# Kernel tuning notes

Measured on AMD Instinct MI355X. Metric: run time of the kernel, lower is better.

## Reference

```python
import jax, jax.numpy as jnp
import numpy as np

NODES_PER_GRAPH = 32
NUM_GRAPHS = 4096
N = NUM_GRAPHS * NODES_PER_GRAPH  # 131072
DEG = 8
E = N * DEG
FEAT = 10


def setup_inputs() -> dict:
    key = jax.random.key(0)
    ks = jax.random.split(key, 32)
    x = jax.random.normal(ks[0], (N, FEAT), dtype=jnp.float32)
    src = jnp.repeat(jnp.arange(N, dtype=jnp.int64), DEG)
    dst = (src // NODES_PER_GRAPH) * NODES_PER_GRAPH + jax.random.randint(
        ks[1], (E,), 0, NODES_PER_GRAPH).astype(jnp.int64)
    edge_index = jnp.stack([src, dst])  # [2, E], row0 = source j, row1 = target i
    batch = (jnp.arange(N, dtype=jnp.int64) // NODES_PER_GRAPH)

    def lin(k, fan_in, shape):
        return jax.random.normal(k, shape, dtype=jnp.float32) / np.sqrt(fan_in)

    inp = dict(x=x, edge_index=edge_index, batch=batch)
    inp['Wq'] = lin(ks[2], 32, (32, 32))
    inp['Wk'] = lin(ks[3], 32, (32, 32))
    inp['Wv'] = lin(ks[4], 32, (32, 32))
    inp['W1'] = lin(ks[5], 10, (10, 64));  inp['a1s'] = lin(ks[6], 16, (4, 16))
    inp['a1d'] = lin(ks[7], 16, (4, 16));  inp['b1'] = jnp.zeros((64,), jnp.float32)
    inp['W2'] = lin(ks[8], 64, (64, 64));  inp['a2s'] = lin(ks[9], 16, (4, 16))
    inp['a2d'] = lin(ks[10], 16, (4, 16)); inp['b2'] = jnp.zeros((64,), jnp.float32)
    inp['W3'] = lin(ks[11], 64, (64, 64)); inp['a3s'] = lin(ks[12], 16, (4, 16))
    inp['a3d'] = lin(ks[13], 16, (4, 16)); inp['b3'] = jnp.zeros((64,), jnp.float32)
    inp['W4'] = lin(ks[14], 64, (64, 64)); inp['a4s'] = lin(ks[15], 64, (1, 64))
    inp['a4d'] = lin(ks[16], 64, (1, 64)); inp['b4'] = jnp.zeros((64,), jnp.float32)
    inp['fcW'] = lin(ks[17], 64, (64, 2)); inp['fcb'] = jnp.zeros((2,), jnp.float32)
    return inp


def gat_conv(x, src, dst, W, a_s, a_d, b, heads, out_c, concat):
    n = x.shape[0]
    h = (x @ W).reshape(n, heads, out_c)                    # [N,H,C]
    e_s = jnp.einsum('nhc,hc->nh', h, a_s)
    e_d = jnp.einsum('nhc,hc->nh', h, a_d)
    e = jax.nn.leaky_relu(e_s[src] + e_d[dst], 0.2)          # [E,H]
    e_max = jax.ops.segment_max(e, dst, num_segments=n)
    e = jnp.exp(e - e_max[dst])
    denom = jax.ops.segment_sum(e, dst, num_segments=n)
    alpha = e / (denom[dst] + 1e-16)                         # softmax per target node
    msg = h[src] * alpha[:, :, None]                         # [E,H,C]
    out = jax.ops.segment_sum(msg, dst, num_segments=n)      # [N,H,C]
    out = out.reshape(n, heads * out_c) if concat else out.mean(axis=1)
    return out + b


def forward(x, edge_index, batch, Wq, Wk, Wv, W1, a1s, a1d, b1, W2, a2s, a2d, b2,
            W3, a3s, a3d, b3, W4, a4s, a4d, b4, fcW, fcb):
    n = x.shape[0]
    b = n // NODES_PER_GRAPH
    # Attention_Layer1: (b*32, 10) -> (b, 10, 32)
    att_in = x.reshape(b, NODES_PER_GRAPH, FEAT).transpose(0, 2, 1)  # [b, sl=10, 32]
    Q = att_in @ Wq
    K = att_in @ Wk
    V = att_in @ Wv
    alpha = jax.nn.softmax(jnp.einsum('bsi,bti->bst', Q, K), axis=2)
    out = jnp.einsum('bst,bti->bsi', alpha, V)               # [b, 10, 32]
    # rearrange 'b i sl -> (b sl) i' with i=10, sl=32
    xg = out.transpose(0, 2, 1).reshape(n, FEAT)             # [(b*32), 10]
    # add self-loops (PyG GATConv default)
    loops = jnp.arange(n, dtype=edge_index.dtype)
    src = jnp.concatenate([edge_index[0], loops])
    dst = jnp.concatenate([edge_index[1], loops])
    xg = jax.nn.leaky_relu(gat_conv(xg, src, dst, W1, a1s, a1d, b1, 4, 16, True), 0.01)
    xg = jax.nn.leaky_relu(gat_conv(xg, src, dst, W2, a2s, a2d, b2, 4, 16, True), 0.01)
    xg = jax.nn.leaky_relu(gat_conv(xg, src, dst, W3, a3s, a3d, b3, 4, 16, True), 0.01)
    xg = jax.nn.leaky_relu(gat_conv(xg, src, dst, W4, a4s, a4d, b4, 1, 64, True), 0.01)
    # global mean pool per graph
    sums = jax.ops.segment_sum(xg, batch, num_segments=b)
    cnts = jax.ops.segment_sum(jnp.ones((n, 1), xg.dtype), batch, num_segments=b)
    pooled = sums / cnts                                     # [b, 64]
    logits = pooled @ fcW + fcb                              # [b, 2]
    probas = jax.nn.softmax(logits, axis=1)
    return logits, probas


def reference(x, edge_index, batch, Wq, Wk, Wv, W1, a1s, a1d, b1, W2, a2s, a2d, b2,
              W3, a3s, a3d, b3, W4, a4s, a4d, b4, fcW, fcb):
    return forward(x, edge_index, batch, Wq, Wk, Wv, W1, a1s, a1d, b1, W2, a2s, a2d,
                   b2, W3, a3s, a3d, b3, W4, a4s, a4d, b4, fcW, fcb)
```

## Files before the change

### kernel.cpp

```cpp
#include <hip/hip_runtime.h>


#define NGRAPH 4096
#define EDGES  (NGRAPH * 256)
#define NT     256
#define LOG2E  1.4426950408889634f

typedef __attribute__((ext_vector_type(8))) short bf16x8;
typedef __attribute__((ext_vector_type(4))) float f32x4;
typedef __attribute__((ext_vector_type(4))) int   i32x4;

__device__ __forceinline__ unsigned f2u(float x){ union{float f;unsigned u;}c;c.f=x;return c.u; }
__device__ __forceinline__ float u2f(unsigned u){ union{unsigned u;float f;}c;c.u=u;return c.f; }

__device__ __forceinline__ void split2(float x0, float x1, unsigned& dhi, unsigned& dlo){
    const unsigned u0 = f2u(x0), u1 = f2u(x1);
    dhi = (u0 >> 16) | (u1 & 0xffff0000u);
    const float l0 = x0 - u2f(u0 & 0xffff0000u);
    const float l1 = x1 - u2f(u1 & 0xffff0000u);
    dlo = (f2u(l0) >> 16) | (f2u(l1) & 0xffff0000u);
}

__device__ __forceinline__ f32x4 mfma16(i32x4 a, i32x4 b, f32x4 c){
    return __builtin_amdgcn_mfma_f32_16x16x32_bf16(
        __builtin_bit_cast(bf16x8, a), __builtin_bit_cast(bf16x8, b), c, 0, 0, 0);
}

template<int KSTEPS>
__device__ __forceinline__ void gat_layer(
    int tid,
    unsigned short (*xh_in)[72], unsigned short (*xl_in)[72],
    unsigned short (*xh_out)[72], unsigned short (*xl_out)[72],
    unsigned short* hh_w, unsigned short* hl_w, float* esw, float* edw,
    const unsigned int* Ap, const char* __restrict__ ws, int l,
    const float* __restrict__ b_g)
{
    const int lane = tid & 63, w = tid >> 6;
    const int n15 = lane & 15, q = lane >> 4;

    f32x4 hC0 = {0,0,0,0}, hC1 = {0,0,0,0};
    f32x4 eC0 = {0,0,0,0}, eC1 = {0,0,0,0};
#pragma unroll
    for (int ks = 0; ks < KSTEPS; ++ks){
        const unsigned short* wr = (const unsigned short*)(ws + l*16384)
                                   + (w*16 + n15)*64 + ks*32 + q*8;
        const i32x4 bh = *(const i32x4*)wr;
        const i32x4 bl = *(const i32x4*)(wr + 4096);
        const unsigned short* er = (const unsigned short*)(ws + 65536 + l*4096)
                                   + n15*64 + ks*32 + q*8;
        const i32x4 eh = *(const i32x4*)er;
        const i32x4 el = *(const i32x4*)(er + 1024);

        const i32x4 a0h = *(const i32x4*)&xh_in[n15][ks*32 + q*8];
        const i32x4 a0l = *(const i32x4*)&xl_in[n15][ks*32 + q*8];
        hC0 = mfma16(a0h, bh, hC0); hC0 = mfma16(a0h, bl, hC0); hC0 = mfma16(a0l, bh, hC0);
        eC0 = mfma16(a0h, eh, eC0); eC0 = mfma16(a0h, el, eC0); eC0 = mfma16(a0l, eh, eC0);

        const i32x4 a1h = *(const i32x4*)&xh_in[16 + n15][ks*32 + q*8];
        const i32x4 a1l = *(const i32x4*)&xl_in[16 + n15][ks*32 + q*8];
        hC1 = mfma16(a1h, bh, hC1); hC1 = mfma16(a1h, bl, hC1); hC1 = mfma16(a1l, bh, hC1);
        eC1 = mfma16(a1h, eh, eC1); eC1 = mfma16(a1h, el, eC1); eC1 = mfma16(a1l, eh, eC1);
    }

    if (n15 == 2*w || n15 == 2*w + 1){
        float* dst = (n15 & 1) ? edw : esw;
#pragma unroll
        for (int r = 0; r < 4; ++r){
            dst[q*4 + r]      = eC0[r];
            dst[16 + q*4 + r] = eC1[r];
        }
    }

#pragma unroll
    for (int mt = 0; mt < 2; ++mt){
        const f32x4 hv = mt ? hC1 : hC0;
        unsigned h0, l0v, h1, l1v;
        split2(hv[0], hv[1], h0, l0v);
        split2(hv[2], hv[3], h1, l1v);
        *(uint2*)&hh_w[n15*40 + mt*16 + q*4] = make_uint2(h0, h1);
        *(uint2*)&hl_w[n15*40 + mt*16 + q*4] = make_uint2(l0v, l1v);
    }

    float pf0[8], pf1[8];
    {
        float es8[8];
        *(float4*)&es8[0] = *(const float4*)&esw[q*8];
        *(float4*)&es8[4] = *(const float4*)&esw[q*8 + 4];
        const float ed0 = edw[n15], ed1 = edw[16 + n15];
        const uint2 c0 = make_uint2(Ap[n15*9 + 2*q], Ap[n15*9 + 2*q + 1]);
        const uint2 c1 = make_uint2(Ap[(16+n15)*9 + 2*q], Ap[(16+n15)*9 + 2*q + 1]);
        float ss0 = 0.f, ss1 = 0.f;
#pragma unroll
        for (int jj = 0; jj < 8; ++jj){
            const unsigned cnt0 = ((jj < 4 ? c0.x >> (8*jj) : c0.y >> (8*(jj-4))) & 0xffu);
            const unsigned cnt1 = ((jj < 4 ? c1.x >> (8*jj) : c1.y >> (8*(jj-4))) & 0xffu);
            float e0 = es8[jj] + ed0; e0 = fmaxf(e0, 0.2f*e0);
            float e1 = es8[jj] + ed1; e1 = fmaxf(e1, 0.2f*e1);
            const float p0 = (float)cnt0 * exp2f(e0);
            const float p1 = (float)cnt1 * exp2f(e1);
            pf0[jj] = p0; ss0 += p0;
            pf1[jj] = p1; ss1 += p1;
        }
        ss0 += __shfl_xor(ss0, 16); ss0 += __shfl_xor(ss0, 32);
        ss1 += __shfl_xor(ss1, 16); ss1 += __shfl_xor(ss1, 32);
        if (q == 0){
            edw[n15]      = 1.f/(ss0 + 1e-16f);
            edw[16 + n15] = 1.f/(ss1 + 1e-16f);
        }
    }

    {
        const i32x4 bh = *(const i32x4*)&hh_w[n15*40 + q*8];
        const i32x4 bl = *(const i32x4*)&hl_w[n15*40 + q*8];
        f32x4 o0 = {0,0,0,0}, o1 = {0,0,0,0};
        i32x4 ph, pl; unsigned th, tl;
#pragma unroll
        for (int r = 0; r < 4; ++r){
            split2(pf0[2*r], pf0[2*r+1], th, tl); ph[r] = (int)th; pl[r] = (int)tl;
        }
        o0 = mfma16(ph, bh, o0); o0 = mfma16(ph, bl, o0); o0 = mfma16(pl, bh, o0);
#pragma unroll
        for (int r = 0; r < 4; ++r){
            split2(pf1[2*r], pf1[2*r+1], th, tl); ph[r] = (int)th; pl[r] = (int)tl;
        }
        o1 = mfma16(ph, bh, o1); o1 = mfma16(ph, bl, o1); o1 = mfma16(pl, bh, o1);

        const float bv = __ldg(b_g + w*16 + n15);
        const f32x4 iv0 = *(const f32x4*)&edw[q*4];
        const f32x4 iv1 = *(const f32x4*)&edw[16 + q*4];
#pragma unroll
        for (int mt = 0; mt < 2; ++mt){
            const f32x4 ov = mt ? o1 : o0;
            const f32x4 iv = mt ? iv1 : iv0;
#pragma unroll
            for (int r = 0; r < 4; ++r){
                const int row = mt*16 + q*4 + r;
                float v = ov[r] * iv[r] + bv;
                v = fmaxf(v, 0.01f*v);
                const unsigned u = f2u(v);
                const float lo = v - u2f(u & 0xffff0000u);
                xh_out[row][w*16 + n15] = (unsigned short)(u >> 16);
                xl_out[row][w*16 + n15] = (unsigned short)(f2u(lo) >> 16);
            }
        }
    }
}

__global__ __launch_bounds__(NT) void gnn_fused(
    const float* __restrict__ x, const int* __restrict__ edge_index,
    const float* __restrict__ b1, const float* __restrict__ b2,
    const float* __restrict__ b3, const float* __restrict__ b4,
    const float* __restrict__ fcW, const float* __restrict__ fcb,
    const char* __restrict__ ws, float* __restrict__ out)
{
    __shared__ __align__(16) unsigned short xap[2][2][32][72];
    __shared__ __align__(16) unsigned short hT[4][2][16][40];
    __shared__ __align__(16) float es_l[4][32];
    __shared__ __align__(16) float ed_l[4][32];
    __shared__ __align__(16) unsigned int Ap[32*9];

    const int g = blockIdx.x, tid = threadIdx.x;
    const int lane = tid & 63, w = tid >> 6;
    const int n15 = lane & 15, q = lane >> 4;

    unsigned short* r0 = &xap[0][0][0][0];
    unsigned short* r1 = &hT[0][0][0][0];

    for (int idx = tid; idx < 288; idx += NT) Ap[idx] = 0u;
    for (int idx = tid; idx < 320; idx += NT){
        const int m = idx / 10, s = idx - 10*m;
        const float v = x[g*320 + idx];
        const unsigned u = f2u(v);
        const float lo = v - u2f(u & 0xffff0000u);
        r0[0   + s*40 + m] = (unsigned short)(u >> 16);
        r0[640 + s*40 + m] = (unsigned short)(f2u(lo) >> 16);
    }
    if (tid < 192){
        const int s = 10 + (tid >> 5), m = tid & 31;
        r0[0   + s*40 + m] = 0;
        r0[640 + s*40 + m] = 0;
    }
    __syncthreads();

    {
        const int* dstp = edge_index + EDGES + g*256;
        const int i = dstp[tid] & 31, j = tid >> 3;
        atomicAdd(&Ap[i*9 + (j >> 2)], 1u << (8*(j & 3)));
        if (tid < 32) atomicAdd(&Ap[tid*9 + (tid >> 2)], 1u << (8*(tid & 3)));
    }
    if (w < 3){
        const unsigned short* wb = (const unsigned short*)(ws + 81920 + w*4096);
        const i32x4 ah = *(const i32x4*)&r0[0   + n15*40 + q*8];
        const i32x4 al = *(const i32x4*)&r0[640 + n15*40 + q*8];
        f32x4 C0 = {0,0,0,0}, C1 = {0,0,0,0};
#pragma unroll
        for (int nt = 0; nt < 2; ++nt){
            const i32x4 bh = *(const i32x4*)&wb[(nt*16 + n15)*32 + q*8];
            const i32x4 bl = *(const i32x4*)&wb[1024 + (nt*16 + n15)*32 + q*8];
            f32x4 acc = nt ? C1 : C0;
            acc = mfma16(ah, bh, acc); acc = mfma16(ah, bl, acc); acc = mfma16(al, bh, acc);
            if (nt) C1 = acc; else C0 = acc;
        }
        if (w < 2){
            const int base = (w == 0) ? 1280 : 2560;
#pragma unroll
            for (int nt = 0; nt < 2; ++nt){
                const f32x4 cv = nt ? C1 : C0;
                const int i = nt*16 + n15;
#pragma unroll
                for (int r = 0; r < 4; ++r){
                    const int s = q*4 + r;
                    const float v = cv[r];
                    const unsigned u = f2u(v);
                    const float lo = v - u2f(u & 0xffff0000u);
                    r0[base + s*40 + i]       = (unsigned short)(u >> 16);
                    r0[base + 640 + s*40 + i] = (unsigned short)(f2u(lo) >> 16);
                }
            }
        } else {
#pragma unroll
            for (int nt = 0; nt < 2; ++nt){
                const f32x4 cv = nt ? C1 : C0;
                const int i = nt*16 + n15;
                unsigned h0, l0v, h1, l1v;
                split2(cv[0], cv[1], h0, l0v);
                split2(cv[2], cv[3], h1, l1v);
                *(uint2*)&r1[0    + i*40 + q*4] = make_uint2(h0, h1);
                *(uint2*)&r1[1280 + i*40 + q*4] = make_uint2(l0v, l1v);
            }
        }
    } else {
        const int plane = lane >> 5, row = lane & 31;
        unsigned short* dst = &r1[plane*1280 + row*40 + 16];
#pragma unroll
        for (int k = 0; k < 4; ++k) *(unsigned long long*)&dst[4*k] = 0ull;
    }
    __syncthreads();

    if (w == 0){
        const i32x4 ah = *(const i32x4*)&r0[1280 + n15*40 + q*8];
        const i32x4 al = *(const i32x4*)&r0[1920 + n15*40 + q*8];
        const i32x4 bh = *(const i32x4*)&r0[2560 + n15*40 + q*8];
        const i32x4 bl = *(const i32x4*)&r0[3200 + n15*40 + q*8];
        f32x4 Sc = {0,0,0,0};
        Sc = mfma16(ah, bh, Sc); Sc = mfma16(ah, bl, Sc); Sc = mfma16(al, bh, Sc);
        const bool valid = (n15 < 10);
#pragma unroll
        for (int r = 0; r < 4; ++r){
            float v = valid ? Sc[r] : -1e30f;
            float m = v;
            m = fmaxf(m, __shfl_xor(m, 1)); m = fmaxf(m, __shfl_xor(m, 2));
            m = fmaxf(m, __shfl_xor(m, 4)); m = fmaxf(m, __shfl_xor(m, 8));
            float p = valid ? exp2f((Sc[r] - m)*LOG2E) : 0.f;
            float s = p;
            s += __shfl_xor(s, 1); s += __shfl_xor(s, 2);
            s += __shfl_xor(s, 4); s += __shfl_xor(s, 8);
            const float sp = p / s;
            const int srow = q*4 + r;
            const unsigned u = f2u(sp);
            const float lo = sp - u2f(u & 0xffff0000u);
            r1[2560 + srow*40 + n15] = (unsigned short)(u >> 16);
            r1[3200 + srow*40 + n15] = (unsigned short)(f2u(lo) >> 16);
            r1[2560 + srow*40 + 16 + n15] = 0;
            r1[3200 + srow*40 + 16 + n15] = 0;
        }
    }
    __syncthreads();

    if (w < 2){
        const i32x4 ah = *(const i32x4*)&r1[2560 + n15*40 + q*8];
        const i32x4 al = *(const i32x4*)&r1[3200 + n15*40 + q*8];
        const i32x4 bh = *(const i32x4*)&r1[0    + (w*16 + n15)*40 + q*8];
        const i32x4 bl = *(const i32x4*)&r1[1280 + (w*16 + n15)*40 + q*8];
        f32x4 O = {0,0,0,0};
        O = mfma16(ah, bh, O); O = mfma16(ah, bl, O); O = mfma16(al, bh, O);
        const int ig = w*16 + n15;
#pragma unroll
        for (int r = 0; r < 4; ++r){
            const int s = q*4 + r;
            if (s < 10){
                const float v = O[r];
                const unsigned u = f2u(v);
                const float lo = v - u2f(u & 0xffff0000u);
                xap[0][0][ig][s] = (unsigned short)(u >> 16);
                xap[0][1][ig][s] = (unsigned short)(f2u(lo) >> 16);
            }
        }
    } else {
        const int idx = tid - 128;
        const int plane = idx >> 6, row = (idx >> 1) & 31, half = idx & 1;
        unsigned short* rowp = &xap[0][plane][row][0];
        if (half == 0){
            *(unsigned*)&rowp[10] = 0u;
#pragma unroll
            for (int c = 0; c < 6; ++c) *(unsigned long long*)&rowp[12 + 4*c] = 0ull;
        } else {
#pragma unroll
            for (int c = 0; c < 7; ++c) *(unsigned long long*)&rowp[36 + 4*c] = 0ull;
        }
    }
    __syncthreads();

    unsigned short* hh_w = &hT[w][0][0][0];
    unsigned short* hl_w = &hT[w][1][0][0];
    float* esw = es_l[w];
    float* edw = ed_l[w];
    gat_layer<1>(tid, xap[0][0], xap[0][1], xap[1][0], xap[1][1], hh_w, hl_w, esw, edw, Ap, ws, 0, b1);
    __syncthreads();
    gat_layer<2>(tid, xap[1][0], xap[1][1], xap[0][0], xap[0][1], hh_w, hl_w, esw, edw, Ap, ws, 1, b2);
    __syncthreads();
    gat_layer<2>(tid, xap[0][0], xap[0][1], xap[1][0], xap[1][1], hh_w, hl_w, esw, edw, Ap, ws, 2, b3);
    __syncthreads();
    gat_layer<2>(tid, xap[1][0], xap[1][1], xap[0][0], xap[0][1], hh_w, hl_w, esw, edw, Ap, ws, 3, b4);
    __syncthreads();

    if (tid < 64){
        float acc = 0.f;
#pragma unroll
        for (int n = 0; n < 32; ++n)
            acc += u2f(((unsigned)xap[0][0][n][tid]) << 16) + u2f(((unsigned)xap[0][1][n][tid]) << 16);
        const float p = acc*(1.f/32.f);
        float c0 = p*__ldg(fcW + 2*tid);
        float c1 = p*__ldg(fcW + 2*tid + 1);
#pragma unroll
        for (int off = 32; off > 0; off >>= 1){
            c0 += __shfl_down(c0, off);
            c1 += __shfl_down(c1, off);
        }
        if (tid == 0){
            const float l0 = c0 + __ldg(fcb), l1 = c1 + __ldg(fcb + 1);
            const float m = fmaxf(l0, l1);
            const float e0 = __expf(l0 - m), e1 = __expf(l1 - m);
            const float inv = 1.f/(e0 + e1);
            out[2*g] = l0;
            out[2*g + 1] = l1;
            out[2*NGRAPH + 2*g] = e0*inv;
            out[2*NGRAPH + 2*g + 1] = e1*inv;
        }
    }
}

__global__ void prep(
    const float* __restrict__ W1, const float* __restrict__ W2,
    const float* __restrict__ W3, const float* __restrict__ W4,
    const float* __restrict__ a1s, const float* __restrict__ a1d,
    const float* __restrict__ a2s, const float* __restrict__ a2d,
    const float* __restrict__ a3s, const float* __restrict__ a3d,
    const float* __restrict__ a4s, const float* __restrict__ a4d,
    const float* __restrict__ Wq, const float* __restrict__ Wk,
    const float* __restrict__ Wv,
    char* __restrict__ ws)
{
    const int b = blockIdx.x, tid = threadIdx.x;
    const float* Wl[4] = {W1, W2, W3, W4};
    const int Kl[4] = {10, 64, 64, 64};
    if (b < 32){
        const int l = b >> 3;
        const float* W = Wl[l];
        const int K = Kl[l];
        unsigned short* hi = (unsigned short*)(ws + l*16384);
        unsigned short* lo = hi + 4096;
        const int base = (b & 7)*512;
        for (int idx = base + tid; idx < base + 512; idx += NT){
            const int n = idx >> 6, k = idx & 63;
            const float v = (k < K) ? __ldg(W + k*64 + n) : 0.f;
            const unsigned u = f2u(v);
            const float lof = v - u2f(u & 0xffff0000u);
            hi[idx] = (unsigned short)(u >> 16);
            lo[idx] = (unsigned short)(f2u(lof) >> 16);
        }
    } else if (b < 36){
        const int l = b - 32;
        const float* W = Wl[l];
        const int K = Kl[l];
        const float* asp[4] = {a1s, a2s, a3s, a4s};
        const float* adp[4] = {a1d, a2d, a3d, a4d};
        const int C = (l < 3) ? 16 : 64;
        unsigned short* basep = (unsigned short*)(ws + 65536 + l*4096);
        for (int idx = tid; idx < 1024; idx += NT){
            const int n = idx >> 6, k = idx & 63;
            float val = 0.f;
            if (n < 8 && k < K){
                const int hh = (l < 3) ? (n >> 1) : 0;
                const float* av = (n & 1) ? adp[l] : asp[l];
                float s = 0.f;
                for (int c = 0; c < C; ++c)
                    s += __ldg(W + k*64 + hh*C + c) * __ldg(av + hh*C + c);
                val = s * LOG2E;
            }
            const unsigned u = f2u(val);
            const float lof = val - u2f(u & 0xffff0000u);
            basep[idx]        = (unsigned short)(u >> 16);
            basep[1024 + idx] = (unsigned short)(f2u(lof) >> 16);
        }
    } else {
        const int mat = b - 36;
        const float* W = (mat == 0) ? Wq : ((mat == 1) ? Wk : Wv);
        unsigned short* hi = (unsigned short*)(ws + 81920 + mat*4096);
        unsigned short* lo = hi + 1024;
        for (int idx = tid; idx < 1024; idx += NT){
            const int i = idx >> 5, m = idx & 31;
            const float v = __ldg(W + m*32 + i);
            const unsigned u = f2u(v);
            const float lof = v - u2f(u & 0xffff0000u);
            hi[idx] = (unsigned short)(u >> 16);
            lo[idx] = (unsigned short)(f2u(lof) >> 16);
        }
    }
}

extern "C" void kernel_launch(void* const* d_in, const int* in_sizes, int n_in,
                              void* d_out, int out_size, void* d_ws, size_t ws_size,
                              hipStream_t stream) {
    (void)in_sizes; (void)n_in; (void)ws_size; (void)out_size;
    prep<<<39, NT, 0, stream>>>(
        (const float*)d_in[6], (const float*)d_in[10], (const float*)d_in[14], (const float*)d_in[18],
        (const float*)d_in[7], (const float*)d_in[8],
        (const float*)d_in[11], (const float*)d_in[12],
        (const float*)d_in[15], (const float*)d_in[16],
        (const float*)d_in[19], (const float*)d_in[20],
        (const float*)d_in[3], (const float*)d_in[4], (const float*)d_in[5],
        (char*)d_ws);
    gnn_fused<<<NGRAPH, NT, 0, stream>>>(
        (const float*)d_in[0], (const int*)d_in[1],
        (const float*)d_in[9], (const float*)d_in[13], (const float*)d_in[17], (const float*)d_in[21],
        (const float*)d_in[22], (const float*)d_in[23],
        (const char*)d_ws, (float*)d_out);
}
```

Before: 200.5 us.

## Process one graph per wavefront, removing block-wide barriers

Changes the work split so each 64-lane wavefront handles a whole graph, with four graphs per 256-thread block, instead of four wavefronts sharing one graph. Each wave now computes all four head tiles of every GAT layer and the whole attention preamble on its own, so every __syncthreads is gone and shared-memory state becomes per-wave. The adjacency count packing also moves from 8-bit to 4-bit fields to shrink the per-graph shared footprint. The cost is more serial MFMA work and more registers per wave, plus a small risk of count overflow if a node has more than 15 duplicate edges to the same neighbour.

```diff
diff --git a/kernel.cpp b/kernel.cpp
--- a/kernel.cpp
+++ b/kernel.cpp
@@ -4,6 +4,7 @@
 #define NGRAPH 4096
 #define EDGES  (NGRAPH * 256)
 #define NT     256
+#define GPB    4
 #define LOG2E  1.4426950408889634f
 
 typedef __attribute__((ext_vector_type(8))) short bf16x8;
@@ -28,90 +29,104 @@
 
 template<int KSTEPS>
 __device__ __forceinline__ void gat_layer(
-    int tid,
-    unsigned short (*xh_in)[72], unsigned short (*xl_in)[72],
-    unsigned short (*xh_out)[72], unsigned short (*xl_out)[72],
-    unsigned short* hh_w, unsigned short* hl_w, float* esw, float* edw,
+    int lane, unsigned short* sw, float* esb, float* edb,
     const unsigned int* Ap, const char* __restrict__ ws, int l,
     const float* __restrict__ b_g)
 {
-    const int lane = tid & 63, w = tid >> 6;
     const int n15 = lane & 15, q = lane >> 4;
-
-    f32x4 hC0 = {0,0,0,0}, hC1 = {0,0,0,0};
+    unsigned short* xaH = sw;
+    unsigned short* xaL = sw + 2304;
+    unsigned short* hTH = sw + 4608;
+    unsigned short* hTL = sw + 5248;
+
+    f32x4 hC0[4], hC1[4];
     f32x4 eC0 = {0,0,0,0}, eC1 = {0,0,0,0};
 #pragma unroll
+    for (int nt = 0; nt < 4; ++nt){
+        hC0[nt] = (f32x4){0,0,0,0};
+        hC1[nt] = (f32x4){0,0,0,0};
+    }
+#pragma unroll
     for (int ks = 0; ks < KSTEPS; ++ks){
-        const unsigned short* wr = (const unsigned short*)(ws + l*16384)
-                                   + (w*16 + n15)*64 + ks*32 + q*8;
-        const i32x4 bh = *(const i32x4*)wr;
-        const i32x4 bl = *(const i32x4*)(wr + 4096);
+        const i32x4 a0h = *(const i32x4*)&xaH[n15*72 + ks*32 + q*8];
+        const i32x4 a0l = *(const i32x4*)&xaL[n15*72 + ks*32 + q*8];
+        const i32x4 a1h = *(const i32x4*)&xaH[(16+n15)*72 + ks*32 + q*8];
+        const i32x4 a1l = *(const i32x4*)&xaL[(16+n15)*72 + ks*32 + q*8];
+
         const unsigned short* er = (const unsigned short*)(ws + 65536 + l*4096)
                                    + n15*64 + ks*32 + q*8;
         const i32x4 eh = *(const i32x4*)er;
         const i32x4 el = *(const i32x4*)(er + 1024);
-
-        const i32x4 a0h = *(const i32x4*)&xh_in[n15][ks*32 + q*8];
-        const i32x4 a0l = *(const i32x4*)&xl_in[n15][ks*32 + q*8];
-        hC0 = mfma16(a0h, bh, hC0); hC0 = mfma16(a0h, bl, hC0); hC0 = mfma16(a0l, bh, hC0);
         eC0 = mfma16(a0h, eh, eC0); eC0 = mfma16(a0h, el, eC0); eC0 = mfma16(a0l, eh, eC0);
-
-        const i32x4 a1h = *(const i32x4*)&xh_in[16 + n15][ks*32 + q*8];
-        const i32x4 a1l = *(const i32x4*)&xl_in[16 + n15][ks*32 + q*8];
-        hC1 = mfma16(a1h, bh, hC1); hC1 = mfma16(a1h, bl, hC1); hC1 = mfma16(a1l, bh, hC1);
         eC1 = mfma16(a1h, eh, eC1); eC1 = mfma16(a1h, el, eC1); eC1 = mfma16(a1l, eh, eC1);
-    }
-
-    if (n15 == 2*w || n15 == 2*w + 1){
-        float* dst = (n15 & 1) ? edw : esw;
+
+#pragma unroll
+        for (int nt = 0; nt < 4; ++nt){
+            const unsigned short* wr = (const unsigned short*)(ws + l*16384)
+                                       + (nt*16 + n15)*64 + ks*32 + q*8;
+            const i32x4 bh = *(const i32x4*)wr;
+            const i32x4 bl = *(const i32x4*)(wr + 4096);
+            hC0[nt] = mfma16(a0h, bh, hC0[nt]);
+            hC0[nt] = mfma16(a0h, bl, hC0[nt]);
+            hC0[nt] = mfma16(a0l, bh, hC0[nt]);
+            hC1[nt] = mfma16(a1h, bh, hC1[nt]);
+            hC1[nt] = mfma16(a1h, bl, hC1[nt]);
+            hC1[nt] = mfma16(a1l, bh, hC1[nt]);
+        }
+    }
+
+    if (n15 < 8){
+        float* dst = (n15 & 1) ? edb : esb;
+        const int h = n15 >> 1;
 #pragma unroll
         for (int r = 0; r < 4; ++r){
-            dst[q*4 + r]      = eC0[r];
-            dst[16 + q*4 + r] = eC1[r];
-        }
-    }
-
-#pragma unroll
-    for (int mt = 0; mt < 2; ++mt){
-        const f32x4 hv = mt ? hC1 : hC0;
-        unsigned h0, l0v, h1, l1v;
-        split2(hv[0], hv[1], h0, l0v);
-        split2(hv[2], hv[3], h1, l1v);
-        *(uint2*)&hh_w[n15*40 + mt*16 + q*4] = make_uint2(h0, h1);
-        *(uint2*)&hl_w[n15*40 + mt*16 + q*4] = make_uint2(l0v, l1v);
-    }
-
-    float pf0[8], pf1[8];
-    {
-        float es8[8];
-        *(float4*)&es8[0] = *(const float4*)&esw[q*8];
-        *(float4*)&es8[4] = *(const float4*)&esw[q*8 + 4];
-        const float ed0 = edw[n15], ed1 = edw[16 + n15];
-        const uint2 c0 = make_uint2(Ap[n15*9 + 2*q], Ap[n15*9 + 2*q + 1]);
-        const uint2 c1 = make_uint2(Ap[(16+n15)*9 + 2*q], Ap[(16+n15)*9 + 2*q + 1]);
-        float ss0 = 0.f, ss1 = 0.f;
-#pragma unroll
-        for (int jj = 0; jj < 8; ++jj){
-            const unsigned cnt0 = ((jj < 4 ? c0.x >> (8*jj) : c0.y >> (8*(jj-4))) & 0xffu);
-            const unsigned cnt1 = ((jj < 4 ? c1.x >> (8*jj) : c1.y >> (8*(jj-4))) & 0xffu);
-            float e0 = es8[jj] + ed0; e0 = fmaxf(e0, 0.2f*e0);
-            float e1 = es8[jj] + ed1; e1 = fmaxf(e1, 0.2f*e1);
-            const float p0 = (float)cnt0 * exp2f(e0);
-            const float p1 = (float)cnt1 * exp2f(e1);
-            pf0[jj] = p0; ss0 += p0;
-            pf1[jj] = p1; ss1 += p1;
-        }
-        ss0 += __shfl_xor(ss0, 16); ss0 += __shfl_xor(ss0, 32);
-        ss1 += __shfl_xor(ss1, 16); ss1 += __shfl_xor(ss1, 32);
-        if (q == 0){
-            edw[n15]      = 1.f/(ss0 + 1e-16f);
-            edw[16 + n15] = 1.f/(ss1 + 1e-16f);
-        }
-    }
-
-    {
-        const i32x4 bh = *(const i32x4*)&hh_w[n15*40 + q*8];
-        const i32x4 bl = *(const i32x4*)&hl_w[n15*40 + q*8];
+            dst[h*32 + q*4 + r]      = eC0[r];
+            dst[h*32 + 16 + q*4 + r] = eC1[r];
+        }
+    }
+
+#pragma unroll
+    for (int nt = 0; nt < 4; ++nt){
+#pragma unroll
+        for (int mt = 0; mt < 2; ++mt){
+            const f32x4 hv = mt ? hC1[nt] : hC0[nt];
+            unsigned h0, l0v, h1, l1v;
+            split2(hv[0], hv[1], h0, l0v);
+            split2(hv[2], hv[3], h1, l1v);
+            *(uint2*)&hTH[n15*40 + mt*16 + q*4] = make_uint2(h0, h1);
+            *(uint2*)&hTL[n15*40 + mt*16 + q*4] = make_uint2(l0v, l1v);
+        }
+
+        float pf0[8], pf1[8];
+        {
+            float es8[8];
+            *(float4*)&es8[0] = *(const float4*)&esb[nt*32 + q*8];
+            *(float4*)&es8[4] = *(const float4*)&esb[nt*32 + q*8 + 4];
+            const float ed0 = edb[nt*32 + n15], ed1 = edb[nt*32 + 16 + n15];
+            const unsigned c0w = Ap[n15*5 + q];
+            const unsigned c1w = Ap[(16+n15)*5 + q];
+            float ss0 = 0.f, ss1 = 0.f;
+#pragma unroll
+            for (int jj = 0; jj < 8; ++jj){
+                const unsigned cnt0 = (c0w >> (4*jj)) & 0xfu;
+                const unsigned cnt1 = (c1w >> (4*jj)) & 0xfu;
+                float e0 = es8[jj] + ed0; e0 = fmaxf(e0, 0.2f*e0);
+                float e1 = es8[jj] + ed1; e1 = fmaxf(e1, 0.2f*e1);
+                const float p0 = (float)cnt0 * exp2f(e0);
+                const float p1 = (float)cnt1 * exp2f(e1);
+                pf0[jj] = p0; ss0 += p0;
+                pf1[jj] = p1; ss1 += p1;
+            }
+            ss0 += __shfl_xor(ss0, 16); ss0 += __shfl_xor(ss0, 32);
+            ss1 += __shfl_xor(ss1, 16); ss1 += __shfl_xor(ss1, 32);
+            if (q == 0){
+                edb[nt*32 + n15]      = 1.f/(ss0 + 1e-16f);
+                edb[nt*32 + 16 + n15] = 1.f/(ss1 + 1e-16f);
+            }
+        }
+
+        const i32x4 bh = *(const i32x4*)&hTH[n15*40 + q*8];
+        const i32x4 bl = *(const i32x4*)&hTL[n15*40 + q*8];
         f32x4 o0 = {0,0,0,0}, o1 = {0,0,0,0};
         i32x4 ph, pl; unsigned th, tl;
 #pragma unroll
@@ -125,9 +140,9 @@
         }
         o1 = mfma16(ph, bh, o1); o1 = mfma16(ph, bl, o1); o1 = mfma16(pl, bh, o1);
 
-        const float bv = __ldg(b_g + w*16 + n15);
-        const f32x4 iv0 = *(const f32x4*)&edw[q*4];
-        const f32x4 iv1 = *(const f32x4*)&edw[16 + q*4];
+        const float bv = __ldg(b_g + nt*16 + n15);
+        const f32x4 iv0 = *(const f32x4*)&edb[nt*32 + q*4];
+        const f32x4 iv1 = *(const f32x4*)&edb[nt*32 + 16 + q*4];
 #pragma unroll
         for (int mt = 0; mt < 2; ++mt){
             const f32x4 ov = mt ? o1 : o0;
@@ -135,12 +150,12 @@
 #pragma unroll
             for (int r = 0; r < 4; ++r){
                 const int row = mt*16 + q*4 + r;
-                float v = ov[r] * iv[r] + bv;
+                float v = ov[r]*iv[r] + bv;
                 v = fmaxf(v, 0.01f*v);
                 const unsigned u = f2u(v);
                 const float lo = v - u2f(u & 0xffff0000u);
-                xh_out[row][w*16 + n15] = (unsigned short)(u >> 16);
-                xl_out[row][w*16 + n15] = (unsigned short)(f2u(lo) >> 16);
+                xaH[row*72 + nt*16 + n15] = (unsigned short)(u >> 16);
+                xaL[row*72 + nt*16 + n15] = (unsigned short)(f2u(lo) >> 16);
             }
         }
     }
@@ -153,181 +168,203 @@
     const float* __restrict__ fcW, const float* __restrict__ fcb,
     const char* __restrict__ ws, float* __restrict__ out)
 {
-    __shared__ __align__(16) unsigned short xap[2][2][32][72];
-    __shared__ __align__(16) unsigned short hT[4][2][16][40];
-    __shared__ __align__(16) float es_l[4][32];
-    __shared__ __align__(16) float ed_l[4][32];
-    __shared__ __align__(16) unsigned int Ap[32*9];
-
-    const int g = blockIdx.x, tid = threadIdx.x;
-    const int lane = tid & 63, w = tid >> 6;
+    __shared__ __align__(16) unsigned short sb[GPB][5888];
+    __shared__ __align__(16) float esb_s[GPB][128];
+    __shared__ __align__(16) float edb_s[GPB][128];
+    __shared__ unsigned int Ap_s[GPB][160];
+
+    const int tid = threadIdx.x, lane = tid & 63, w = tid >> 6;
+    const int g = blockIdx.x * GPB + w;
     const int n15 = lane & 15, q = lane >> 4;
 
-    unsigned short* r0 = &xap[0][0][0][0];
-    unsigned short* r1 = &hT[0][0][0][0];
-
-    for (int idx = tid; idx < 288; idx += NT) Ap[idx] = 0u;
-    for (int idx = tid; idx < 320; idx += NT){
+    unsigned short* sw = sb[w];
+    float* esb = esb_s[w];
+    float* edb = edb_s[w];
+    unsigned int* Ap = Ap_s[w];
+
+    Ap[lane] = 0u;
+    Ap[64 + lane] = 0u;
+    if (lane < 32) Ap[128 + lane] = 0u;
+#pragma unroll
+    for (int t = 0; t < 5; ++t){
+        const int idx = lane + t*64;
         const int m = idx / 10, s = idx - 10*m;
         const float v = x[g*320 + idx];
         const unsigned u = f2u(v);
         const float lo = v - u2f(u & 0xffff0000u);
-        r0[0   + s*40 + m] = (unsigned short)(u >> 16);
-        r0[640 + s*40 + m] = (unsigned short)(f2u(lo) >> 16);
-    }
-    if (tid < 192){
-        const int s = 10 + (tid >> 5), m = tid & 31;
-        r0[0   + s*40 + m] = 0;
-        r0[640 + s*40 + m] = 0;
-    }
-    __syncthreads();
+        sw[0   + s*40 + m] = (unsigned short)(u >> 16);
+        sw[640 + s*40 + m] = (unsigned short)(f2u(lo) >> 16);
+    }
+#pragma unroll
+    for (int t = 0; t < 3; ++t){
+        const int idx = lane + t*64;
+        const int s = 10 + (idx >> 5), m = idx & 31;
+        sw[0   + s*40 + m] = 0;
+        sw[640 + s*40 + m] = 0;
+    }
 
     {
         const int* dstp = edge_index + EDGES + g*256;
-        const int i = dstp[tid] & 31, j = tid >> 3;
-        atomicAdd(&Ap[i*9 + (j >> 2)], 1u << (8*(j & 3)));
-        if (tid < 32) atomicAdd(&Ap[tid*9 + (tid >> 2)], 1u << (8*(tid & 3)));
-    }
-    if (w < 3){
-        const unsigned short* wb = (const unsigned short*)(ws + 81920 + w*4096);
-        const i32x4 ah = *(const i32x4*)&r0[0   + n15*40 + q*8];
-        const i32x4 al = *(const i32x4*)&r0[640 + n15*40 + q*8];
-        f32x4 C0 = {0,0,0,0}, C1 = {0,0,0,0};
-#pragma unroll
-        for (int nt = 0; nt < 2; ++nt){
-            const i32x4 bh = *(const i32x4*)&wb[(nt*16 + n15)*32 + q*8];
-            const i32x4 bl = *(const i32x4*)&wb[1024 + (nt*16 + n15)*32 + q*8];
-            f32x4 acc = nt ? C1 : C0;
-            acc = mfma16(ah, bh, acc); acc = mfma16(ah, bl, acc); acc = mfma16(al, bh, acc);
-            if (nt) C1 = acc; else C0 = acc;
-        }
-        if (w < 2){
-            const int base = (w == 0) ? 1280 : 2560;
+        const int4 d4 = *(const int4*)(dstp + lane*4);
+#pragma unroll
+        for (int e = 0; e < 4; ++e){
+            const int dv = (e==0) ? d4.x : (e==1) ? d4.y : (e==2) ? d4.z : d4.w;
+            const int i = dv & 31, j = (lane*4 + e) >> 3;
+            atomicAdd(&Ap[i*5 + (j >> 3)], 1u << (4*(j & 7)));
+        }
+        if (lane < 32) atomicAdd(&Ap[lane*5 + (lane >> 3)], 1u << (4*(lane & 7)));
+    }
+
+    {
+        const i32x4 ah = *(const i32x4*)&sw[0   + n15*40 + q*8];
+        const i32x4 al = *(const i32x4*)&sw[640 + n15*40 + q*8];
+
+#pragma unroll
+        for (int mat = 0; mat < 2; ++mat){
+            const unsigned short* wb = (const unsigned short*)(ws + 81920 + mat*4096);
+            const int obase = 1280 + mat*1280;
 #pragma unroll
             for (int nt = 0; nt < 2; ++nt){
-                const f32x4 cv = nt ? C1 : C0;
+                const i32x4 bh = *(const i32x4*)&wb[(nt*16+n15)*32 + q*8];
+                const i32x4 bl = *(const i32x4*)&wb[1024 + (nt*16+n15)*32 + q*8];
+                f32x4 C = {0,0,0,0};
+                C = mfma16(ah, bh, C); C = mfma16(ah, bl, C); C = mfma16(al, bh, C);
                 const int i = nt*16 + n15;
 #pragma unroll
                 for (int r = 0; r < 4; ++r){
                     const int s = q*4 + r;
-                    const float v = cv[r];
+                    const float v = C[r];
                     const unsigned u = f2u(v);
                     const float lo = v - u2f(u & 0xffff0000u);
-                    r0[base + s*40 + i]       = (unsigned short)(u >> 16);
-                    r0[base + 640 + s*40 + i] = (unsigned short)(f2u(lo) >> 16);
+                    sw[obase + s*40 + i]       = (unsigned short)(u >> 16);
+                    sw[obase + 640 + s*40 + i] = (unsigned short)(f2u(lo) >> 16);
                 }
             }
-        } else {
+        }
+
+        f32x4 VC[2];
+        {
+            const unsigned short* wb = (const unsigned short*)(ws + 81920 + 2*4096);
 #pragma unroll
             for (int nt = 0; nt < 2; ++nt){
-                const f32x4 cv = nt ? C1 : C0;
-                const int i = nt*16 + n15;
-                unsigned h0, l0v, h1, l1v;
-                split2(cv[0], cv[1], h0, l0v);
-                split2(cv[2], cv[3], h1, l1v);
-                *(uint2*)&r1[0    + i*40 + q*4] = make_uint2(h0, h1);
-                *(uint2*)&r1[1280 + i*40 + q*4] = make_uint2(l0v, l1v);
-            }
-        }
-    } else {
-        const int plane = lane >> 5, row = lane & 31;
-        unsigned short* dst = &r1[plane*1280 + row*40 + 16];
-#pragma unroll
-        for (int k = 0; k < 4; ++k) *(unsigned long long*)&dst[4*k] = 0ull;
-    }
-    __syncthreads();
-
-    if (w == 0){
-        const i32x4 ah = *(const i32x4*)&r0[1280 + n15*40 + q*8];
-        const i32x4 al = *(const i32x4*)&r0[1920 + n15*40 + q*8];
-        const i32x4 bh = *(const i32x4*)&r0[2560 + n15*40 + q*8];
-        const i32x4 bl = *(const i32x4*)&r0[3200 + n15*40 + q*8];
-        f32x4 Sc = {0,0,0,0};
-        Sc = mfma16(ah, bh, Sc); Sc = mfma16(ah, bl, Sc); Sc = mfma16(al, bh, Sc);
-        const bool valid = (n15 < 10);
-#pragma unroll
-        for (int r = 0; r < 4; ++r){
-            float v = valid ? Sc[r] : -1e30f;
-            float m = v;
-            m = fmaxf(m, __shfl_xor(m, 1)); m = fmaxf(m, __shfl_xor(m, 2));
-            m = fmaxf(m, __shfl_xor(m, 4)); m = fmaxf(m, __shfl_xor(m, 8));
-            float p = valid ? exp2f((Sc[r] - m)*LOG2E) : 0.f;
-            float s = p;
-            s += __shfl_xor(s, 1); s += __shfl_xor(s, 2);
-            s += __shfl_xor(s, 4); s += __shfl_xor(s, 8);
-            const float sp = p / s;
-            const int srow = q*4 + r;
-            const unsigned u = f2u(sp);
-            const float lo = sp - u2f(u & 0xffff0000u);
-            r1[2560 + srow*40 + n15] = (unsigned short)(u >> 16);
-            r1[3200 + srow*40 + n15] = (unsigned short)(f2u(lo) >> 16);
-            r1[2560 + srow*40 + 16 + n15] = 0;
-            r1[3200 + srow*40 + 16 + n15] = 0;
-        }
-    }
-    __syncthreads();
-
-    if (w < 2){
-        const i32x4 ah = *(const i32x4*)&r1[2560 + n15*40 + q*8];
-        const i32x4 al = *(const i32x4*)&r1[3200 + n15*40 + q*8];
-        const i32x4 bh = *(const i32x4*)&r1[0    + (w*16 + n15)*40 + q*8];
-        const i32x4 bl = *(const i32x4*)&r1[1280 + (w*16 + n15)*40 + q*8];
-        f32x4 O = {0,0,0,0};
-        O = mfma16(ah, bh, O); O = mfma16(ah, bl, O); O = mfma16(al, bh, O);
-        const int ig = w*16 + n15;
-#pragma unroll
-        for (int r = 0; r < 4; ++r){
-            const int s = q*4 + r;
-            if (s < 10){
-                const float v = O[r];
-                const unsigned u = f2u(v);
-                const float lo = v - u2f(u & 0xffff0000u);
-                xap[0][0][ig][s] = (unsigned short)(u >> 16);
-                xap[0][1][ig][s] = (unsigned short)(f2u(lo) >> 16);
-            }
-        }
-    } else {
-        const int idx = tid - 128;
-        const int plane = idx >> 6, row = (idx >> 1) & 31, half = idx & 1;
-        unsigned short* rowp = &xap[0][plane][row][0];
-        if (half == 0){
-            *(unsigned*)&rowp[10] = 0u;
-#pragma unroll
-            for (int c = 0; c < 6; ++c) *(unsigned long long*)&rowp[12 + 4*c] = 0ull;
-        } else {
-#pragma unroll
-            for (int c = 0; c < 7; ++c) *(unsigned long long*)&rowp[36 + 4*c] = 0ull;
-        }
-    }
-    __syncthreads();
-
-    unsigned short* hh_w = &hT[w][0][0][0];
-    unsigned short* hl_w = &hT[w][1][0][0];
-    float* esw = es_l[w];
-    float* edw = ed_l[w];
-    gat_layer<1>(tid, xap[0][0], xap[0][1], xap[1][0], xap[1][1], hh_w, hl_w, esw, edw, Ap, ws, 0, b1);
-    __syncthreads();
-    gat_layer<2>(tid, xap[1][0], xap[1][1], xap[0][0], xap[0][1], hh_w, hl_w, esw, edw, Ap, ws, 1, b2);
-    __syncthreads();
-    gat_layer<2>(tid, xap[0][0], xap[0][1], xap[1][0], xap[1][1], hh_w, hl_w, esw, edw, Ap, ws, 2, b3);
-    __syncthreads();
-    gat_layer<2>(tid, xap[1][0], xap[1][1], xap[0][0], xap[0][1], hh_w, hl_w, esw, edw, Ap, ws, 3, b4);
-    __syncthreads();
-
-    if (tid < 64){
+                const i32x4 bh = *(const i32x4*)&wb[(nt*16+n15)*32 + q*8];
+                const i32x4 bl = *(const i32x4*)&wb[1024 + (nt*16+n15)*32 + q*8];
+                f32x4 C = {0,0,0,0};
+                C = mfma16(ah, bh, C); C = mfma16(ah, bl, C); C = mfma16(al, bh, C);
+                VC[nt] = C;
+            }
+        }
+
+        {
+            const i32x4 qh = *(const i32x4*)&sw[1280 + n15*40 + q*8];
+            const i32x4 ql = *(const i32x4*)&sw[1920 + n15*40 + q*8];
+            const i32x4 kh = *(const i32x4*)&sw[2560 + n15*40 + q*8];
+            const i32x4 kl = *(const i32x4*)&sw[3200 + n15*40 + q*8];
+            f32x4 Sc = {0,0,0,0};
+            Sc = mfma16(qh, kh, Sc); Sc = mfma16(qh, kl, Sc); Sc = mfma16(ql, kh, Sc);
+            const bool valid = (n15 < 10);
+#pragma unroll
+            for (int r = 0; r < 4; ++r){
+                float v = valid ? Sc[r] : -1e30f;
+                float m = v;
+                m = fmaxf(m, __shfl_xor(m, 1)); m = fmaxf(m, __shfl_xor(m, 2));
+                m = fmaxf(m, __shfl_xor(m, 4)); m = fmaxf(m, __shfl_xor(m, 8));
+                float p = valid ? exp2f((Sc[r] - m)*LOG2E) : 0.f;
+                float s = p;
+                s += __shfl_xor(s, 1); s += __shfl_xor(s, 2);
+                s += __shfl_xor(s, 4); s += __shfl_xor(s, 8);
+                const float sp = p / s;
+                const int srow = q*4 + r;
+                const unsigned u = f2u(sp);
+                const float lo = sp - u2f(u & 0xffff0000u);
+                sw[2560 + srow*40 + n15] = (unsigned short)(u >> 16);
+                sw[3200 + srow*40 + n15] = (unsigned short)(f2u(lo) >> 16);
+                sw[2560 + srow*40 + 16 + n15] = 0;
+                sw[3200 + srow*40 + 16 + n15] = 0;
+            }
+        }
+
+#pragma unroll
+        for (int nt = 0; nt < 2; ++nt){
+            const f32x4 cv = VC[nt];
+            const int i = nt*16 + n15;
+            unsigned h0, l0v, h1, l1v;
+            split2(cv[0], cv[1], h0, l0v);
+            split2(cv[2], cv[3], h1, l1v);
+            *(uint2*)&sw[0    + i*40 + q*4] = make_uint2(h0, h1);
+            *(uint2*)&sw[1280 + i*40 + q*4] = make_uint2(l0v, l1v);
+        }
+        {
+            const int i2 = lane >> 1, half = lane & 1;
+            const int b0 = i2*40 + 16 + half*8;
+            *(unsigned long long*)&sw[b0]          = 0ull;
+            *(unsigned long long*)&sw[b0 + 4]      = 0ull;
+            *(unsigned long long*)&sw[1280 + b0]   = 0ull;
+            *(unsigned long long*)&sw[1280 + b0+4] = 0ull;
+        }
+
+        f32x4 O[2];
+        {
+            const i32x4 sh = *(const i32x4*)&sw[2560 + n15*40 + q*8];
+            const i32x4 sl = *(const i32x4*)&sw[3200 + n15*40 + q*8];
+#pragma unroll
+            for (int nt = 0; nt < 2; ++nt){
+                const i32x4 vh = *(const i32x4*)&sw[0    + (nt*16+n15)*40 + q*8];
+                const i32x4 vl = *(const i32x4*)&sw[1280 + (nt*16+n15)*40 + q*8];
+                f32x4 C = {0,0,0,0};
+                C = mfma16(sh, vh, C); C = mfma16(sh, vl, C); C = mfma16(sl, vh, C);
+                O[nt] = C;
+            }
+        }
+#pragma unroll
+        for (int nt = 0; nt < 2; ++nt){
+            const int i = nt*16 + n15;
+#pragma unroll
+            for (int r = 0; r < 4; ++r){
+                const int s = q*4 + r;
+                if (s < 10){
+                    const float v = O[nt][r];
+                    const unsigned u = f2u(v);
+                    const float lo = v - u2f(u & 0xffff0000u);
+                    sw[i*72 + s]        = (unsigned short)(u >> 16);
+                    sw[2304 + i*72 + s] = (unsigned short)(f2u(lo) >> 16);
+                }
+            }
+        }
+#pragma unroll
+        for (int p = 0; p < 2; ++p){
+            unsigned short* rowp = sw + p*2304 + (lane >> 1)*72;
+            if ((lane & 1) == 0){
+                *(unsigned*)&rowp[10] = 0u;
+#pragma unroll
+                for (int c = 0; c < 6; ++c) *(unsigned long long*)&rowp[12 + 4*c] = 0ull;
+            } else {
+#pragma unroll
+                for (int c = 0; c < 7; ++c) *(unsigned long long*)&rowp[36 + 4*c] = 0ull;
+            }
+        }
+    }
+
+    gat_layer<1>(lane, sw, esb, edb, Ap, ws, 0, b1);
+    gat_layer<2>(lane, sw, esb, edb, Ap, ws, 1, b2);
+    gat_layer<2>(lane, sw, esb, edb, Ap, ws, 2, b3);
+    gat_layer<2>(lane, sw, esb, edb, Ap, ws, 3, b4);
+
+    {
         float acc = 0.f;
 #pragma unroll
         for (int n = 0; n < 32; ++n)
-            acc += u2f(((unsigned)xap[0][0][n][tid]) << 16) + u2f(((unsigned)xap[0][1][n][tid]) << 16);
+            acc += u2f(((unsigned)sw[n*72 + lane]) << 16)
+                 + u2f(((unsigned)sw[2304 + n*72 + lane]) << 16);
         const float p = acc*(1.f/32.f);
-        float c0 = p*__ldg(fcW + 2*tid);
-        float c1 = p*__ldg(fcW + 2*tid + 1);
+        float c0 = p*__ldg(fcW + 2*lane);
+        float c1 = p*__ldg(fcW + 2*lane + 1);
 #pragma unroll
         for (int off = 32; off > 0; off >>= 1){
             c0 += __shfl_down(c0, off);
             c1 += __shfl_down(c1, off);
         }
-        if (tid == 0){
+        if (lane == 0){
             const float l0 = c0 + __ldg(fcb), l1 = c1 + __ldg(fcb + 1);
             const float m = fmaxf(l0, l1);
             const float e0 = __expf(l0 - m), e1 = __expf(l1 - m);
@@ -421,7 +458,7 @@
         (const float*)d_in[19], (const float*)d_in[20],
         (const float*)d_in[3], (const float*)d_in[4], (const float*)d_in[5],
         (char*)d_ws);
-    gnn_fused<<<NGRAPH, NT, 0, stream>>>(
+    gnn_fused<<<NGRAPH / GPB, NT, 0, stream>>>(
         (const float*)d_in[0], (const int*)d_in[1],
         (const float*)d_in[9], (const float*)d_in[13], (const float*)d_in[17], (const float*)d_in[21],
         (const float*)d_in[22], (const float*)d_in[23],
```

New measurement: 190.6 us. -4.9%, faster.
